# Performance work log

Measured on AMD Instinct MI355X. Metric: run time of the kernel, lower is better.

The kernel has to match this reference:

```python
import jax, jax.numpy as jnp
import numpy as np

D_MODEL = 1024
NUM_HEADS = 16
D_K = D_MODEL // NUM_HEADS
BATCH = 2
SEQ = 2048
NEG = -1e9


def _xavier(key, shape):
    fan_in, fan_out = shape[1], shape[0]
    a = np.sqrt(6.0 / (fan_in + fan_out)).astype(np.float32)
    return jax.random.uniform(key, shape, jnp.float32, -a, a)


def setup_inputs() -> dict:
    key = jax.random.key(0)
    kx, kq, kk, kv, ko = jax.random.split(key, 5)
    x = jax.random.normal(kx, (BATCH, SEQ, D_MODEL), jnp.float32)
    # additive causal mask: 0 on/below diagonal, -1e9 above
    causal = jnp.tril(jnp.ones((SEQ, SEQ), jnp.bool_))
    mask = jnp.where(causal, 0.0, NEG).astype(jnp.float32)
    # nn.Linear weights are (out, in); y = x @ W.T
    return {
        "x": x,
        "mask": mask,
        "W_q": _xavier(kq, (D_MODEL, D_MODEL)),
        "W_k": _xavier(kk, (D_MODEL, D_MODEL)),
        "W_v": _xavier(kv, (D_MODEL, D_MODEL)),
        "W_o": _xavier(ko, (D_MODEL, D_MODEL)),
    }


def reference(x, mask, W_q, W_k, W_v, W_o):
    B, S, _ = x.shape
    scale = 1.0 / np.sqrt(D_K).astype(np.float32)

    def split_heads(t):  # (B,S,D) -> (B,H,S,d_k)
        return t.reshape(B, S, NUM_HEADS, D_K).transpose(0, 2, 1, 3)

    Q = split_heads(x @ W_q.T)
    K = split_heads(x @ W_k.T)
    V = split_heads(x @ W_v.T)
    # (B,H,S,S) score matrix, as in the original (no flash fusion)
    scores = jnp.einsum("bhqd,bhkd->bhqk", Q, K) * scale
    scores = scores + mask[None, None, :, :]
    attn = jax.nn.softmax(scores, axis=-1)
    out = jnp.einsum("bhqk,bhkd->bhqd", attn, V)
    out = out.transpose(0, 2, 1, 3).reshape(B, S, D_MODEL)
    return out @ W_o.T
```

## Files before the change

### kernel.cpp

```cpp
#include <hip/hip_runtime.h>
#include <hip/hip_bf16.h>
#include <cstdint>

typedef __attribute__((ext_vector_type(8))) short bf16x8;
typedef __attribute__((ext_vector_type(4))) float f32x4;
typedef unsigned short u16;

#define D_MODEL 1024
#define NHEADS 16
#define DKH 64
#define BATCH 2
#define SEQ 2048
#define MTOT (BATCH * SEQ)

__device__ __forceinline__ u16 f2bf(float f) {
    union { float f; uint32_t u; } v; v.f = f;
    uint32_t r = (v.u + 0x7fffu + ((v.u >> 16) & 1u)) >> 16;
    return (u16)r;
}
__device__ __forceinline__ float fexp2(float x) {
    float r; asm("v_exp_f32 %0, %1" : "=v"(r) : "v"(x)); return r;
}
__device__ __forceinline__ uint32_t cvtpk(float lo, float hi) {
    uint32_t r; asm("v_cvt_pk_bf16_f32 %0, %1, %2" : "=v"(r) : "v"(lo), "v"(hi)); return r;
}

__global__ void cvt_all(const float* __restrict__ x,
                        const float* __restrict__ wq, const float* __restrict__ wk,
                        const float* __restrict__ wv, const float* __restrict__ wo,
                        u16* __restrict__ out) {
    int i = blockIdx.x * blockDim.x + threadIdx.x;
    const float* src; int off;
    if (i < 524288) { src = x; off = i; }
    else {
        int k = i - 524288; int w = k >> 17; off = k & 131071;
        src = (w == 0) ? wq : (w == 1) ? wk : (w == 2) ? wv : wo;
    }
    const float4* p = (const float4*)src + (size_t)off * 2;
    float4 a = p[0], b = p[1];
    bf16x8 o;
    o[0] = (short)f2bf(a.x); o[1] = (short)f2bf(a.y);
    o[2] = (short)f2bf(a.z); o[3] = (short)f2bf(a.w);
    o[4] = (short)f2bf(b.x); o[5] = (short)f2bf(b.y);
    o[6] = (short)f2bf(b.z); o[7] = (short)f2bf(b.w);
    *(bf16x8*)(out + (size_t)i * 8) = o;
}

__global__ __launch_bounds__(256) void gemm_qkv(const u16* __restrict__ A,
                                                const u16* __restrict__ Bt,
                                                u16* __restrict__ Qo,
                                                u16* __restrict__ Ko,
                                                u16* __restrict__ Vto, float qscale) {
    __shared__ __align__(16) u16 SH[17408];
    u16* As = SH;
    u16* Bs = SH + 8192;
    const int K = 1024;
    const int tid = threadIdx.x;
    const int wid = tid >> 6, lane = tid & 63;
    const int ln = lane & 15, hq = lane >> 4;
    const int wr = wid >> 1, wc = wid & 1;
    const int m0 = blockIdx.y * 128, n0 = blockIdx.x * 128;
    const int l8r = lane >> 3, l8c = (lane & 7) * 8;

    f32x4 acc[4][4] = {};

    for (int k0 = 0; k0 < K; k0 += 64) {
#pragma unroll
        for (int it = 0; it < 4; ++it) {
            int chunk = wid * 4 + it;
            int r = chunk * 8 + l8r;
            __builtin_amdgcn_global_load_lds(
                (const __attribute__((address_space(1))) void*)(A + (size_t)(m0 + r) * K + k0 + l8c),
                (__attribute__((address_space(3))) void*)(As + chunk * 512), 16, 0, 0);
            __builtin_amdgcn_global_load_lds(
                (const __attribute__((address_space(1))) void*)(Bt + (size_t)(n0 + r) * K + k0 + l8c),
                (__attribute__((address_space(3))) void*)(Bs + chunk * 512), 16, 0, 0);
        }
        asm volatile("s_waitcnt vmcnt(0)" ::: "memory");
        __syncthreads();
#pragma unroll
        for (int kk = 0; kk < 64; kk += 32) {
            bf16x8 af[4], bfr[4];
#pragma unroll
            for (int s = 0; s < 4; ++s) {
                af[s]  = *(const bf16x8*)(As + (wr * 64 + s * 16 + ln) * 64 + kk + 8 * hq);
                bfr[s] = *(const bf16x8*)(Bs + (wc * 64 + s * 16 + ln) * 64 + kk + 8 * hq);
            }
#pragma unroll
            for (int i = 0; i < 4; ++i)
#pragma unroll
                for (int j = 0; j < 4; ++j)
                    acc[i][j] = __builtin_amdgcn_mfma_f32_16x16x32_bf16(af[i], bfr[j], acc[i][j], 0, 0, 0);
        }
        __syncthreads();
    }

    if (n0 < 2048) {
        u16* out = (n0 < 1024) ? Qo : Ko;
        const int nb = (n0 < 1024) ? n0 : n0 - 1024;
        const float scale = (n0 < 1024) ? qscale : 1.0f;
#pragma unroll
        for (int i = 0; i < 4; ++i) {
            int row = m0 + wr * 64 + i * 16 + hq * 4;
#pragma unroll
            for (int j = 0; j < 4; ++j) {
                int col = nb + wc * 64 + j * 16 + ln;
#pragma unroll
                for (int q = 0; q < 4; ++q)
                    out[(size_t)(row + q) * 1024 + col] = f2bf(acc[i][j][q] * scale);
            }
        }
    } else {
#pragma unroll
        for (int i = 0; i < 4; ++i) {
            int rl = wr * 64 + i * 16 + hq * 4;
#pragma unroll
            for (int j = 0; j < 4; ++j) {
                int cl = wc * 64 + j * 16 + ln;
                ushort4 v;
                v.x = f2bf(acc[i][j][0]); v.y = f2bf(acc[i][j][1]);
                v.z = f2bf(acc[i][j][2]); v.w = f2bf(acc[i][j][3]);
                *(ushort4*)(SH + cl * 136 + rl) = v;
            }
        }
        __syncthreads();
        const int dbase = n0 - 2048;
#pragma unroll
        for (int it = 0; it < 16; ++it) {
            int lc = wid * 32 + it * 2 + (lane >> 5);
            int lr = (lane & 31) * 4;
            ushort4 v = *(const ushort4*)(SH + lc * 136 + lr);
            *(ushort4*)(Vto + (size_t)(dbase + lc) * MTOT + m0 + lr) = v;
        }
    }
}

__global__ __launch_bounds__(256) void gemm_o(const u16* __restrict__ A,
                                              const u16* __restrict__ Bt,
                                              float* __restrict__ C) {
    __shared__ __align__(16) u16 As[64 * 64];
    __shared__ __align__(16) u16 Bs[128 * 64];
    const int K = 1024;
    const int tid = threadIdx.x;
    const int wid = tid >> 6, lane = tid & 63;
    const int ln = lane & 15, hq = lane >> 4;
    const int wr = wid >> 1, wc = wid & 1;
    const int m0 = blockIdx.y * 64, n0 = blockIdx.x * 128;
    const int l8r = lane >> 3, l8c = (lane & 7) * 8;

    f32x4 acc[2][4] = {};

    for (int k0 = 0; k0 < K; k0 += 64) {
#pragma unroll
        for (int it = 0; it < 6; ++it) {
            int chunk = wid * 6 + it;
            if (chunk < 8) {
                int r = chunk * 8 + l8r;
                __builtin_amdgcn_global_load_lds(
                    (const __attribute__((address_space(1))) void*)(A + (size_t)(m0 + r) * K + k0 + l8c),
                    (__attribute__((address_space(3))) void*)(As + chunk * 512), 16, 0, 0);
            } else {
                int c2 = chunk - 8;
                int r = c2 * 8 + l8r;
                __builtin_amdgcn_global_load_lds(
                    (const __attribute__((address_space(1))) void*)(Bt + (size_t)(n0 + r) * K + k0 + l8c),
                    (__attribute__((address_space(3))) void*)(Bs + c2 * 512), 16, 0, 0);
            }
        }
        asm volatile("s_waitcnt vmcnt(0)" ::: "memory");
        __syncthreads();
#pragma unroll
        for (int kk = 0; kk < 64; kk += 32) {
            bf16x8 af[2], bfr[4];
#pragma unroll
            for (int s = 0; s < 2; ++s)
                af[s] = *(const bf16x8*)(As + (wr * 32 + s * 16 + ln) * 64 + kk + 8 * hq);
#pragma unroll
            for (int j = 0; j < 4; ++j)
                bfr[j] = *(const bf16x8*)(Bs + (wc * 64 + j * 16 + ln) * 64 + kk + 8 * hq);
#pragma unroll
            for (int s = 0; s < 2; ++s)
#pragma unroll
                for (int j = 0; j < 4; ++j)
                    acc[s][j] = __builtin_amdgcn_mfma_f32_16x16x32_bf16(af[s], bfr[j], acc[s][j], 0, 0, 0);
        }
        __syncthreads();
    }

#pragma unroll
    for (int s = 0; s < 2; ++s) {
        int row = m0 + wr * 32 + s * 16 + hq * 4;
#pragma unroll
        for (int j = 0; j < 4; ++j) {
            int col = n0 + wc * 64 + j * 16 + ln;
#pragma unroll
            for (int q = 0; q < 4; ++q)
                C[(size_t)(row + q) * 1024 + col] = acc[s][j][q];
        }
    }
}

__device__ __forceinline__ void stage_k(u16* __restrict__ dst, const u16* __restrict__ src,
                                        int kv, int wid, int lane) {
#pragma unroll
    for (int r = 0; r < 2; ++r) {
        int base = r * 2048 + wid * 512;
        int s = (base + lane * 8) >> 6;
        int d = ((lane & 7) ^ (s & 7)) << 3;
        __builtin_amdgcn_global_load_lds(
            (const __attribute__((address_space(1))) void*)(src + (size_t)(kv * 64 + s) * D_MODEL + d),
            (__attribute__((address_space(3))) void*)(dst + base), 16, 0, 0);
    }
}
__device__ __forceinline__ void stage_v(u16* __restrict__ dst, const u16* __restrict__ src,
                                        int kv, int wid, int lane) {
#pragma unroll
    for (int r = 0; r < 2; ++r) {
        int base = r * 2048 + wid * 512;
        int dd = (base + lane * 8) >> 6;
        int sc = ((lane & 7) ^ (dd & 7)) << 3;
        __builtin_amdgcn_global_load_lds(
            (const __attribute__((address_space(1))) void*)(src + (size_t)dd * MTOT + kv * 64 + sc),
            (__attribute__((address_space(3))) void*)(dst + base), 16, 0, 0);
    }
}

__global__ __launch_bounds__(256) void flash_attn(const u16* __restrict__ Q,
                                                  const u16* __restrict__ Kg,
                                                  const u16* __restrict__ Vt,
                                                  u16* __restrict__ O) {
    __shared__ __align__(16) u16 Ks[2][4096];
    __shared__ __align__(16) u16 Vs[2][4096];
    __shared__ __align__(16) u16 Pl[4][1024];
    const int tid = threadIdx.x, wid = tid >> 6, lane = tid & 63;
    const int ln = lane & 15, hq = lane >> 4;
    u16* Pw = Pl[wid];
    const int bid = blockIdx.x;
    const int xcd = bid & 7, s0 = bid >> 3;
    const int t = 31 - (s0 >> 2);
    const int bh = xcd * 4 + (s0 & 3);
    const int b = bh >> 4, h = bh & 15;
    const int qs0 = t * 64 + wid * 16;
    const int NT = t + 1;

    const u16* Kb = Kg + (size_t)(b * SEQ) * D_MODEL + h * DKH;
    const u16* Vb = Vt + (size_t)(h * DKH) * MTOT + b * SEQ;

    const u16* Qp = Q + (size_t)(b * SEQ + qs0 + ln) * D_MODEL + h * DKH;
    bf16x8 qf0 = *(const bf16x8*)(Qp + hq * 8);
    bf16x8 qf1 = *(const bf16x8*)(Qp + 32 + hq * 8);

    f32x4 oacc[4] = {};
    float m = -INFINITY, l = 0.f;

    stage_k(Ks[0], Kb, 0, wid, lane);
    stage_v(Vs[0], Vb, 0, wid, lane);
    asm volatile("s_waitcnt vmcnt(0)" ::: "memory");
    __builtin_amdgcn_s_barrier();

    for (int kv = 0; kv < NT; ++kv) {
        const int cur = kv & 1;
        if (kv + 1 < NT) {
            stage_k(Ks[cur ^ 1], Kb, kv + 1, wid, lane);
            stage_v(Vs[cur ^ 1], Vb, kv + 1, wid, lane);
        }
        const int diag = (kv == t);
        const u16* Kc = Ks[cur];
        const u16* Vc = Vs[cur];
        bf16x8 ka[4][2], va[4][2];
#pragma unroll
        for (int c = 0; c < 4; ++c)
#pragma unroll
            for (int kh = 0; kh < 2; ++kh) {
                int row = c * 16 + ln;
                int slot = ((kh * 4 + hq) ^ (ln & 7)) << 3;
                ka[c][kh] = *(const bf16x8*)(Kc + row * 64 + slot);
                va[c][kh] = *(const bf16x8*)(Vc + row * 64 + slot);
            }
        f32x4 st[4];
        __builtin_amdgcn_s_setprio(1);
#pragma unroll
        for (int c = 0; c < 4; ++c) {
            if (diag && c > wid) { st[c] = f32x4{-1e30f, -1e30f, -1e30f, -1e30f}; continue; }
            f32x4 z = {};
            z = __builtin_amdgcn_mfma_f32_16x16x32_bf16(ka[c][0], qf0, z, 0, 0, 0);
            st[c] = __builtin_amdgcn_mfma_f32_16x16x32_bf16(ka[c][1], qf1, z, 0, 0, 0);
        }
        __builtin_amdgcn_s_setprio(0);
        if (diag) {
#pragma unroll
            for (int j4 = 0; j4 < 4; ++j4)
                if (hq * 4 + j4 > ln) st[wid][j4] = -1e30f;
        }
        float rm = fmaxf(fmaxf(fmaxf(st[0][0], st[0][1]), fmaxf(st[0][2], st[0][3])),
                         fmaxf(fmaxf(st[1][0], st[1][1]), fmaxf(st[1][2], st[1][3])));
        float rm2 = fmaxf(fmaxf(fmaxf(st[2][0], st[2][1]), fmaxf(st[2][2], st[2][3])),
                          fmaxf(fmaxf(st[3][0], st[3][1]), fmaxf(st[3][2], st[3][3])));
        rm = fmaxf(rm, rm2);
        rm = fmaxf(rm, __shfl_xor(rm, 16));
        rm = fmaxf(rm, __shfl_xor(rm, 32));

        if (!__all(rm <= m)) {
            float mn = fmaxf(m, rm);
            float al = fexp2(m - mn);
            m = mn;
            l *= al;
#pragma unroll
            for (int t4 = 0; t4 < 4; ++t4)
#pragma unroll
                for (int j4 = 0; j4 < 4; ++j4) oacc[t4][j4] *= al;
        }
        float rs = 0.f;
#pragma unroll
        for (int c = 0; c < 4; ++c)
#pragma unroll
            for (int j4 = 0; j4 < 4; ++j4) {
                float pv = fexp2(st[c][j4] - m);
                st[c][j4] = pv;
                rs += pv;
            }
        rs += __shfl_xor(rs, 16);
        rs += __shfl_xor(rs, 32);
        l += rs;

#pragma unroll
        for (int c = 0; c < 4; ++c) {
            uint2 w;
            w.x = cvtpk(st[c][0], st[c][1]);
            w.y = cvtpk(st[c][2], st[c][3]);
            int col = (c * 16 + hq * 4) ^ ((ln & 7) << 3);
            *(uint2*)(Pw + ln * 64 + col) = w;
        }
        bf16x8 pb0 = *(const bf16x8*)(Pw + ln * 64 + ((hq * 8) ^ ((ln & 7) << 3)));
        bf16x8 pb1 = *(const bf16x8*)(Pw + ln * 64 + ((32 + hq * 8) ^ ((ln & 7) << 3)));
        __builtin_amdgcn_s_setprio(1);
#pragma unroll
        for (int t4 = 0; t4 < 4; ++t4) {
            oacc[t4] = __builtin_amdgcn_mfma_f32_16x16x32_bf16(va[t4][0], pb0, oacc[t4], 0, 0, 0);
            oacc[t4] = __builtin_amdgcn_mfma_f32_16x16x32_bf16(va[t4][1], pb1, oacc[t4], 0, 0, 0);
        }
        __builtin_amdgcn_s_setprio(0);
        if (kv + 1 < NT) {
            asm volatile("s_waitcnt vmcnt(0)" ::: "memory");
            __builtin_amdgcn_s_barrier();
        }
    }

    float inv = 1.0f / l;
    u16* Op = O + (size_t)(b * SEQ + qs0 + ln) * D_MODEL + h * DKH;
#pragma unroll
    for (int t4 = 0; t4 < 4; ++t4) {
        ushort4 v;
        v.x = f2bf(oacc[t4][0] * inv);
        v.y = f2bf(oacc[t4][1] * inv);
        v.z = f2bf(oacc[t4][2] * inv);
        v.w = f2bf(oacc[t4][3] * inv);
        *(ushort4*)(Op + t4 * 16 + hq * 4) = v;
    }
}

extern "C" void kernel_launch(void* const* d_in, const int* in_sizes, int n_in,
                              void* d_out, int out_size, void* d_ws, size_t ws_size,
                              hipStream_t stream) {
    const float* x  = (const float*)d_in[0];
    const float* Wq = (const float*)d_in[2];
    const float* Wk = (const float*)d_in[3];
    const float* Wv = (const float*)d_in[4];
    const float* Wo = (const float*)d_in[5];

    u16* ws  = (u16*)d_ws;
    u16* xb  = ws;
    u16* Wqb = xb + 4194304;
    u16* Wob = Wqb + 3145728;
    u16* Qb  = Wob + 1048576;
    u16* Kb  = Qb + 4194304;
    u16* Vtb = Kb + 4194304;
    u16* Ob  = Vtb + 4194304;

    cvt_all<<<4096, 256, 0, stream>>>(x, Wq, Wk, Wv, Wo, ws);

    const float QSCALE = 0.125f * 1.4426950408889634f;
    gemm_qkv<<<dim3(24, 32), 256, 0, stream>>>(xb, Wqb, Qb, Kb, Vtb, QSCALE);

    flash_attn<<<dim3(1024), 256, 0, stream>>>(Qb, Kb, Vtb, Ob);

    gemm_o<<<dim3(8, 64), 256, 0, stream>>>(Ob, Wob, (float*)d_out);
}
```

Measured before the change: 125.3 us.

## Double-buffer LDS and XOR-swizzle tiles in QKV and output projection GEMMs

New measurement: 105.2 us (median of 3 runs). 16.0% less time.

```diff
diff --git a/kernel.cpp b/kernel.cpp
--- a/kernel.cpp
+++ b/kernel.cpp
@@ -51,40 +51,52 @@
                                                 u16* __restrict__ Qo,
                                                 u16* __restrict__ Ko,
                                                 u16* __restrict__ Vto, float qscale) {
-    __shared__ __align__(16) u16 SH[17408];
-    u16* As = SH;
-    u16* Bs = SH + 8192;
+    __shared__ __align__(16) u16 SH[32768];
     const int K = 1024;
     const int tid = threadIdx.x;
     const int wid = tid >> 6, lane = tid & 63;
     const int ln = lane & 15, hq = lane >> 4;
     const int wr = wid >> 1, wc = wid & 1;
-    const int m0 = blockIdx.y * 128, n0 = blockIdx.x * 128;
-    const int l8r = lane >> 3, l8c = (lane & 7) * 8;
+    const int bx = (blockIdx.x + 16) % 24;
+    const int m0 = blockIdx.y * 128, n0 = bx * 128;
+    const int l8r = lane >> 3;
+    const int swsrc = ((lane & 7) ^ l8r) << 3;
+    const int rsw = (ln & 7);
+
+#define QKV_STAGE(aoff, k0)                                                            \
+    {                                                                                  \
+        _Pragma("unroll")                                                              \
+        for (int it = 0; it < 4; ++it) {                                               \
+            int chunk = wid * 4 + it;                                                  \
+            int r = chunk * 8 + l8r;                                                   \
+            __builtin_amdgcn_global_load_lds(                                          \
+                (const __attribute__((address_space(1))) void*)(A + (size_t)(m0 + r) * K + (k0) + swsrc), \
+                (__attribute__((address_space(3))) void*)(SH + (aoff) + chunk * 512), 16, 0, 0); \
+            __builtin_amdgcn_global_load_lds(                                          \
+                (const __attribute__((address_space(1))) void*)(Bt + (size_t)(n0 + r) * K + (k0) + swsrc), \
+                (__attribute__((address_space(3))) void*)(SH + 16384 + (aoff) + chunk * 512), 16, 0, 0); \
+        }                                                                              \
+    }
 
     f32x4 acc[4][4] = {};
 
-    for (int k0 = 0; k0 < K; k0 += 64) {
-#pragma unroll
-        for (int it = 0; it < 4; ++it) {
-            int chunk = wid * 4 + it;
-            int r = chunk * 8 + l8r;
-            __builtin_amdgcn_global_load_lds(
-                (const __attribute__((address_space(1))) void*)(A + (size_t)(m0 + r) * K + k0 + l8c),
-                (__attribute__((address_space(3))) void*)(As + chunk * 512), 16, 0, 0);
-            __builtin_amdgcn_global_load_lds(
-                (const __attribute__((address_space(1))) void*)(Bt + (size_t)(n0 + r) * K + k0 + l8c),
-                (__attribute__((address_space(3))) void*)(Bs + chunk * 512), 16, 0, 0);
-        }
-        asm volatile("s_waitcnt vmcnt(0)" ::: "memory");
-        __syncthreads();
+    QKV_STAGE(0, 0);
+    asm volatile("s_waitcnt vmcnt(0)" ::: "memory");
+    __builtin_amdgcn_s_barrier();
+
+    for (int t = 0; t < 16; ++t) {
+        const int aoff = (t & 1) * 8192;
+        if (t < 15) QKV_STAGE(aoff ^ 8192, (t + 1) * 64);
+        const u16* As = SH + aoff;
+        const u16* Bs = SH + 16384 + aoff;
 #pragma unroll
         for (int kk = 0; kk < 64; kk += 32) {
+            const int slot = (kk >> 3) + hq;
             bf16x8 af[4], bfr[4];
 #pragma unroll
             for (int s = 0; s < 4; ++s) {
-                af[s]  = *(const bf16x8*)(As + (wr * 64 + s * 16 + ln) * 64 + kk + 8 * hq);
-                bfr[s] = *(const bf16x8*)(Bs + (wc * 64 + s * 16 + ln) * 64 + kk + 8 * hq);
+                af[s]  = *(const bf16x8*)(As + (wr * 64 + s * 16 + ln) * 64 + ((slot ^ rsw) << 3));
+                bfr[s] = *(const bf16x8*)(Bs + (wc * 64 + s * 16 + ln) * 64 + ((slot ^ rsw) << 3));
             }
 #pragma unroll
             for (int i = 0; i < 4; ++i)
@@ -92,7 +104,10 @@
                 for (int j = 0; j < 4; ++j)
                     acc[i][j] = __builtin_amdgcn_mfma_f32_16x16x32_bf16(af[i], bfr[j], acc[i][j], 0, 0, 0);
         }
-        __syncthreads();
+        if (t < 15) {
+            asm volatile("s_waitcnt vmcnt(0)" ::: "memory");
+            __builtin_amdgcn_s_barrier();
+        }
     }
 
     if (n0 < 2048) {
@@ -111,6 +126,7 @@
             }
         }
     } else {
+        __syncthreads();
 #pragma unroll
         for (int i = 0; i < 4; ++i) {
             int rl = wr * 64 + i * 16 + hq * 4;
@@ -138,53 +154,69 @@
 __global__ __launch_bounds__(256) void gemm_o(const u16* __restrict__ A,
                                               const u16* __restrict__ Bt,
                                               float* __restrict__ C) {
-    __shared__ __align__(16) u16 As[64 * 64];
-    __shared__ __align__(16) u16 Bs[128 * 64];
+    __shared__ __align__(16) u16 SH2[24576];
     const int K = 1024;
     const int tid = threadIdx.x;
     const int wid = tid >> 6, lane = tid & 63;
     const int ln = lane & 15, hq = lane >> 4;
     const int wr = wid >> 1, wc = wid & 1;
     const int m0 = blockIdx.y * 64, n0 = blockIdx.x * 128;
-    const int l8r = lane >> 3, l8c = (lane & 7) * 8;
+    const int l8r = lane >> 3;
+    const int swsrc = ((lane & 7) ^ l8r) << 3;
+    const int rsw = (ln & 7);
+
+#define GO_STAGE(aoff, boff, k0)                                                       \
+    {                                                                                  \
+        _Pragma("unroll")                                                              \
+        for (int it = 0; it < 2; ++it) {                                               \
+            int chunk = wid * 2 + it;                                                  \
+            int r = chunk * 8 + l8r;                                                   \
+            __builtin_amdgcn_global_load_lds(                                          \
+                (const __attribute__((address_space(1))) void*)(A + (size_t)(m0 + r) * K + (k0) + swsrc), \
+                (__attribute__((address_space(3))) void*)(SH2 + (aoff) + chunk * 512), 16, 0, 0); \
+        }                                                                              \
+        _Pragma("unroll")                                                              \
+        for (int it = 0; it < 4; ++it) {                                               \
+            int chunk = wid * 4 + it;                                                  \
+            int r = chunk * 8 + l8r;                                                   \
+            __builtin_amdgcn_global_load_lds(                                          \
+                (const __attribute__((address_space(1))) void*)(Bt + (size_t)(n0 + r) * K + (k0) + swsrc), \
+                (__attribute__((address_space(3))) void*)(SH2 + 8192 + (boff) + chunk * 512), 16, 0, 0); \
+        }                                                                              \
+    }
 
     f32x4 acc[2][4] = {};
 
-    for (int k0 = 0; k0 < K; k0 += 64) {
-#pragma unroll
-        for (int it = 0; it < 6; ++it) {
-            int chunk = wid * 6 + it;
-            if (chunk < 8) {
-                int r = chunk * 8 + l8r;
-                __builtin_amdgcn_global_load_lds(
-                    (const __attribute__((address_space(1))) void*)(A + (size_t)(m0 + r) * K + k0 + l8c),
-                    (__attribute__((address_space(3))) void*)(As + chunk * 512), 16, 0, 0);
-            } else {
-                int c2 = chunk - 8;
-                int r = c2 * 8 + l8r;
-                __builtin_amdgcn_global_load_lds(
-                    (const __attribute__((address_space(1))) void*)(Bt + (size_t)(n0 + r) * K + k0 + l8c),
-                    (__attribute__((address_space(3))) void*)(Bs + c2 * 512), 16, 0, 0);
-            }
-        }
-        asm volatile("s_waitcnt vmcnt(0)" ::: "memory");
-        __syncthreads();
+    GO_STAGE(0, 0, 0);
+    asm volatile("s_waitcnt vmcnt(0)" ::: "memory");
+    __builtin_amdgcn_s_barrier();
+
+    for (int t = 0; t < 16; ++t) {
+        const int aoff = (t & 1) * 4096;
+        const int boff = (t & 1) * 8192;
+        if (t < 15) GO_STAGE(aoff ^ 4096, boff ^ 8192, (t + 1) * 64);
+        const u16* As = SH2 + aoff;
+        const u16* Bs = SH2 + 8192 + boff;
 #pragma unroll
         for (int kk = 0; kk < 64; kk += 32) {
+            const int slot = (kk >> 3) + hq;
             bf16x8 af[2], bfr[4];
 #pragma unroll
             for (int s = 0; s < 2; ++s)
-                af[s] = *(const bf16x8*)(As + (wr * 32 + s * 16 + ln) * 64 + kk + 8 * hq);
+                af[s] = *(const bf16x8*)(As + (wr * 32 + s * 16 + ln) * 64 + ((slot ^ rsw) << 3));
 #pragma unroll
             for (int j = 0; j < 4; ++j)
-                bfr[j] = *(const bf16x8*)(Bs + (wc * 64 + j * 16 + ln) * 64 + kk + 8 * hq);
+                bfr[j] = *(const bf16x8*)(Bs + (wc * 64 + j * 16 + ln) * 64 + ((slot ^ rsw) << 3));
 #pragma unroll
             for (int s = 0; s < 2; ++s)
 #pragma unroll
                 for (int j = 0; j < 4; ++j)
                     acc[s][j] = __builtin_amdgcn_mfma_f32_16x16x32_bf16(af[s], bfr[j], acc[s][j], 0, 0, 0);
         }
-        __syncthreads();
+        if (t < 15) {
+            asm volatile("s_waitcnt vmcnt(0)" ::: "memory");
+            __builtin_amdgcn_s_barrier();
+        }
     }
 
 #pragma unroll
```
